# Kernel optimization log

Measured on AMD Instinct MI355X. Metric: run time of the kernel, lower is better.

Reference implementation:

```python
import jax, jax.numpy as jnp
import numpy as np

N_IN = 4_194_304   # len(x)
E = 33_554_432     # len(ptrs) == len(csr)
N_OUT = 4_194_304  # csr[-1] + 1


def setup_inputs() -> dict:
    key = jax.random.key(0)
    kx, kp, kc = jax.random.split(key, 3)
    x = jax.random.normal(kx, (N_IN,), dtype=jnp.float32)
    ptrs = jax.random.randint(kp, (E,), 0, N_IN, dtype=jnp.int32)
    csr = jnp.sort(jax.random.randint(kc, (E,), 0, N_OUT, dtype=jnp.int32))
    # guarantee csr[-1] + 1 == N_OUT (output buffer size in the torch module)
    csr = csr.at[0].set(0).at[-1].set(N_OUT - 1)
    return {"x": x, "ptrs": ptrs, "csr": csr}


def reference(x, ptrs, csr):
    # gather by ptrs, then segment-sum by sorted csr ids into N_OUT buckets
    return jax.ops.segment_sum(x[ptrs], csr, num_segments=N_OUT,
                               indices_are_sorted=True)
```

## Files before the change

kernel.cpp:

```cpp
#include <hip/hip_runtime.h>
#include <hip/hip_fp16.h>


typedef int   v4i __attribute__((ext_vector_type(4)));
typedef float v4f __attribute__((ext_vector_type(4)));

#define VPT   16
#define BLOCK 256

__global__ __launch_bounds__(BLOCK) void x_to_f16_kernel(
    const float* __restrict__ x, __half* __restrict__ xh)
{
    const int i = (blockIdx.x * BLOCK + threadIdx.x) * 8;
    const v4f* src = reinterpret_cast<const v4f*>(x + i);
    v4f a = __builtin_nontemporal_load(src);
    v4f b = __builtin_nontemporal_load(src + 1);
    union { __half h[8]; v4i v; } u;
#pragma unroll
    for (int k = 0; k < 4; ++k) u.h[k]     = __float2half(a[k]);
#pragma unroll
    for (int k = 0; k < 4; ++k) u.h[4 + k] = __float2half(b[k]);
    *reinterpret_cast<v4i*>(xh + i) = u.v;
}

__global__ __launch_bounds__(BLOCK) void seg_sum_f16_kernel(
    const __half* __restrict__ xh,
    const int*    __restrict__ ptrs,
    const int*    __restrict__ csr,
    float*        __restrict__ out)
{
    const long long tid  = (long long)blockIdx.x * BLOCK + threadIdx.x;
    const long long base = tid * VPT;

    const v4i* p4 = reinterpret_cast<const v4i*>(ptrs + base);
    const v4i* c4 = reinterpret_cast<const v4i*>(csr  + base);

    v4i p[VPT / 4], c[VPT / 4];
#pragma unroll
    for (int q = 0; q < VPT / 4; ++q) {
        p[q] = __builtin_nontemporal_load(p4 + q);
        c[q] = __builtin_nontemporal_load(c4 + q);
    }

    int pi[VPT], ci[VPT];
#pragma unroll
    for (int q = 0; q < VPT / 4; ++q) {
#pragma unroll
        for (int k = 0; k < 4; ++k) {
            pi[4 * q + k] = p[q][k];
            ci[4 * q + k] = c[q][k];
        }
    }

    float v[VPT];
#pragma unroll
    for (int j = 0; j < VPT; ++j) v[j] = __half2float(xh[pi[j]]);

    float acc = v[0];
    int   cur = ci[0];
#pragma unroll
    for (int j = 1; j < VPT; ++j) {
        if (ci[j] == cur) {
            acc += v[j];
        } else {
            atomicAdd(&out[cur], acc);
            cur = ci[j];
            acc = v[j];
        }
    }
    atomicAdd(&out[cur], acc);
}

__global__ __launch_bounds__(BLOCK) void seg_sum_f32_kernel(
    const float* __restrict__ x,
    const int*   __restrict__ ptrs,
    const int*   __restrict__ csr,
    float*       __restrict__ out)
{
    const long long tid  = (long long)blockIdx.x * BLOCK + threadIdx.x;
    const long long base = tid * VPT;
    const v4i* p4 = reinterpret_cast<const v4i*>(ptrs + base);
    const v4i* c4 = reinterpret_cast<const v4i*>(csr  + base);
    v4i p[VPT / 4], c[VPT / 4];
#pragma unroll
    for (int q = 0; q < VPT / 4; ++q) {
        p[q] = __builtin_nontemporal_load(p4 + q);
        c[q] = __builtin_nontemporal_load(c4 + q);
    }
    int pi[VPT], ci[VPT];
#pragma unroll
    for (int q = 0; q < VPT / 4; ++q) {
#pragma unroll
        for (int k = 0; k < 4; ++k) { pi[4*q+k] = p[q][k]; ci[4*q+k] = c[q][k]; }
    }
    float v[VPT];
#pragma unroll
    for (int j = 0; j < VPT; ++j) v[j] = x[pi[j]];
    float acc = v[0];
    int   cur = ci[0];
#pragma unroll
    for (int j = 1; j < VPT; ++j) {
        if (ci[j] == cur) { acc += v[j]; }
        else { atomicAdd(&out[cur], acc); cur = ci[j]; acc = v[j]; }
    }
    atomicAdd(&out[cur], acc);
}

extern "C" void kernel_launch(void* const* d_in, const int* in_sizes, int n_in,
                              void* d_out, int out_size, void* d_ws, size_t ws_size,
                              hipStream_t stream) {
    const float* x    = (const float*)d_in[0];
    const int*   ptrs = (const int*)d_in[1];
    const int*   csr  = (const int*)d_in[2];
    float*       out  = (float*)d_out;

    const int n_in_elems = in_sizes[0];
    const int e          = in_sizes[1];
    const int threads    = e / VPT;
    const int grid       = threads / BLOCK;

    hipMemsetAsync(d_out, 0, (size_t)out_size * sizeof(float), stream);

    const size_t xh_bytes = (size_t)n_in_elems * sizeof(__half);
    if (ws_size >= xh_bytes) {
        __half* xh = (__half*)d_ws;
        x_to_f16_kernel<<<n_in_elems / (BLOCK * 8), BLOCK, 0, stream>>>(x, xh);
        seg_sum_f16_kernel<<<grid, BLOCK, 0, stream>>>(xh, ptrs, csr, out);
    } else {
        seg_sum_f32_kernel<<<grid, BLOCK, 0, stream>>>(x, ptrs, csr, out);
    }
}
```

Before: 391.3 us.

## Split gather into two passes over x halves with XCD-aware block remapping

Runs the gather-and-segment-sum kernel twice, each pass only gathering the entries whose pointer falls in one half of the fp16 x array, so the working set of random gathers is smaller and more likely to stay in cache. Blocks are remapped so that consecutive chunks land on the same XCD, improving L2 locality for the streamed index arrays. In exchange, ptrs and csr are read twice from HBM and the number of atomics can nearly double, since each segment may emit one atomic per pass.

New measurement: 454.6 us. +16.2%, slower.

```diff
diff --git a/kernel.cpp b/kernel.cpp
--- a/kernel.cpp
+++ b/kernel.cpp
@@ -7,6 +7,8 @@
 
 #define VPT   16
 #define BLOCK 256
+#define NPASS 2
+#define NXCD  8
 
 __global__ __launch_bounds__(BLOCK) void x_to_f16_kernel(
     const float* __restrict__ x, __half* __restrict__ xh)
@@ -23,14 +25,18 @@
     *reinterpret_cast<v4i*>(xh + i) = u.v;
 }
 
-__global__ __launch_bounds__(BLOCK) void seg_sum_f16_kernel(
+__global__ __launch_bounds__(BLOCK) void seg_sum_pass_kernel(
     const __half* __restrict__ xh,
     const int*    __restrict__ ptrs,
     const int*    __restrict__ csr,
-    float*        __restrict__ out)
+    float*        __restrict__ out,
+    int lo, unsigned wsize)
 {
-    const long long tid  = (long long)blockIdx.x * BLOCK + threadIdx.x;
-    const long long base = tid * VPT;
+    const int nb    = gridDim.x;
+    const int bid   = blockIdx.x;
+    const int chunk = (bid & (NXCD - 1)) * (nb / NXCD) + (bid / NXCD);
+
+    const long long base = ((long long)chunk * BLOCK + threadIdx.x) * VPT;
 
     const v4i* p4 = reinterpret_cast<const v4i*>(ptrs + base);
     const v4i* c4 = reinterpret_cast<const v4i*>(csr  + base);
@@ -52,23 +58,29 @@
         }
     }
 
+    bool  in[VPT];
     float v[VPT];
 #pragma unroll
-    for (int j = 0; j < VPT; ++j) v[j] = __half2float(xh[pi[j]]);
+    for (int j = 0; j < VPT; ++j)
+        in[j] = ((unsigned)(pi[j] - lo) < wsize);
+#pragma unroll
+    for (int j = 0; j < VPT; ++j)
+        v[j] = in[j] ? __half2float(xh[pi[j]]) : 0.0f;
 
-    float acc = v[0];
+    float acc = 0.0f;
     int   cur = ci[0];
+    bool  any = false;
 #pragma unroll
-    for (int j = 1; j < VPT; ++j) {
-        if (ci[j] == cur) {
-            acc += v[j];
-        } else {
-            atomicAdd(&out[cur], acc);
+    for (int j = 0; j < VPT; ++j) {
+        if (ci[j] != cur) {
+            if (any) atomicAdd(&out[cur], acc);
             cur = ci[j];
-            acc = v[j];
+            acc = 0.0f;
+            any = false;
         }
+        if (in[j]) { acc += v[j]; any = true; }
     }
-    atomicAdd(&out[cur], acc);
+    if (any) atomicAdd(&out[cur], acc);
 }
 
 __global__ __launch_bounds__(BLOCK) void seg_sum_f32_kernel(
@@ -122,10 +134,14 @@
     hipMemsetAsync(d_out, 0, (size_t)out_size * sizeof(float), stream);
 
     const size_t xh_bytes = (size_t)n_in_elems * sizeof(__half);
-    if (ws_size >= xh_bytes) {
+    if (ws_size >= xh_bytes && (grid % NXCD) == 0) {
         __half* xh = (__half*)d_ws;
         x_to_f16_kernel<<<n_in_elems / (BLOCK * 8), BLOCK, 0, stream>>>(x, xh);
-        seg_sum_f16_kernel<<<grid, BLOCK, 0, stream>>>(xh, ptrs, csr, out);
+        const unsigned wsize = (unsigned)(n_in_elems / NPASS);
+        for (int pass = 0; pass < NPASS; ++pass) {
+            seg_sum_pass_kernel<<<grid, BLOCK, 0, stream>>>(
+                xh, ptrs, csr, out, pass * (int)wsize, wsize);
+        }
     } else {
         seg_sum_f32_kernel<<<grid, BLOCK, 0, stream>>>(x, ptrs, csr, out);
     }
```

## Double per-thread work and remap blocks to XCD-contiguous chunks in fp16 segsum

Applied to the files above, without the earlier changes.

Each thread in the fp16 path now handles 32 edges instead of 16, halving the grid. Blocks are remapped so that blocks landing on the same XCD (round-robin dispatch) process contiguous ranges of ptrs/csr, aiming to improve L2 locality of output atomics and cross-block segment boundaries. Gathers now load raw ushort values and convert lazily. Register pressure doubles, which can lower occupancy and reduce gather latency hiding.

New measurement: 474.9 us. 1.21x slower.

```diff
diff --git a/kernel.cpp b/kernel.cpp
--- a/kernel.cpp
+++ b/kernel.cpp
@@ -5,8 +5,10 @@
 typedef int   v4i __attribute__((ext_vector_type(4)));
 typedef float v4f __attribute__((ext_vector_type(4)));
 
-#define VPT   16
+#define VPT   32
+#define HALF_VPT 16
 #define BLOCK 256
+#define NXCD  8
 
 __global__ __launch_bounds__(BLOCK) void x_to_f16_kernel(
     const float* __restrict__ x, __half* __restrict__ xh)
@@ -29,11 +31,16 @@
     const int*    __restrict__ csr,
     float*        __restrict__ out)
 {
-    const long long tid  = (long long)blockIdx.x * BLOCK + threadIdx.x;
-    const long long base = tid * VPT;
+    const int nb    = gridDim.x;
+    const int bid   = blockIdx.x;
+    const int chunk = (bid & (NXCD - 1)) * (nb / NXCD) + (bid / NXCD);
+
+    const long long base = ((long long)chunk * BLOCK + threadIdx.x) * VPT;
 
     const v4i* p4 = reinterpret_cast<const v4i*>(ptrs + base);
     const v4i* c4 = reinterpret_cast<const v4i*>(csr  + base);
+    const unsigned short* __restrict__ xu =
+        reinterpret_cast<const unsigned short*>(xh);
 
     v4i p[VPT / 4], c[VPT / 4];
 #pragma unroll
@@ -52,20 +59,21 @@
         }
     }
 
-    float v[VPT];
+    unsigned short h[VPT];
 #pragma unroll
-    for (int j = 0; j < VPT; ++j) v[j] = __half2float(xh[pi[j]]);
+    for (int j = 0; j < VPT; ++j) h[j] = xu[pi[j]];
 
-    float acc = v[0];
+    float acc = __half2float(__ushort_as_half(h[0]));
     int   cur = ci[0];
 #pragma unroll
     for (int j = 1; j < VPT; ++j) {
+        const float vj = __half2float(__ushort_as_half(h[j]));
         if (ci[j] == cur) {
-            acc += v[j];
+            acc += vj;
         } else {
             atomicAdd(&out[cur], acc);
             cur = ci[j];
-            acc = v[j];
+            acc = vj;
         }
     }
     atomicAdd(&out[cur], acc);
@@ -78,28 +86,28 @@
     float*       __restrict__ out)
 {
     const long long tid  = (long long)blockIdx.x * BLOCK + threadIdx.x;
-    const long long base = tid * VPT;
+    const long long base = tid * HALF_VPT;
     const v4i* p4 = reinterpret_cast<const v4i*>(ptrs + base);
     const v4i* c4 = reinterpret_cast<const v4i*>(csr  + base);
-    v4i p[VPT / 4], c[VPT / 4];
+    v4i p[HALF_VPT / 4], c[HALF_VPT / 4];
 #pragma unroll
-    for (int q = 0; q < VPT / 4; ++q) {
+    for (int q = 0; q < HALF_VPT / 4; ++q) {
         p[q] = __builtin_nontemporal_load(p4 + q);
         c[q] = __builtin_nontemporal_load(c4 + q);
     }
-    int pi[VPT], ci[VPT];
+    int pi[HALF_VPT], ci[HALF_VPT];
 #pragma unroll
-    for (int q = 0; q < VPT / 4; ++q) {
+    for (int q = 0; q < HALF_VPT / 4; ++q) {
 #pragma unroll
         for (int k = 0; k < 4; ++k) { pi[4*q+k] = p[q][k]; ci[4*q+k] = c[q][k]; }
     }
-    float v[VPT];
+    float v[HALF_VPT];
 #pragma unroll
-    for (int j = 0; j < VPT; ++j) v[j] = x[pi[j]];
+    for (int j = 0; j < HALF_VPT; ++j) v[j] = x[pi[j]];
     float acc = v[0];
     int   cur = ci[0];
 #pragma unroll
-    for (int j = 1; j < VPT; ++j) {
+    for (int j = 1; j < HALF_VPT; ++j) {
         if (ci[j] == cur) { acc += v[j]; }
         else { atomicAdd(&out[cur], acc); cur = ci[j]; acc = v[j]; }
     }
@@ -116,17 +124,17 @@
 
     const int n_in_elems = in_sizes[0];
     const int e          = in_sizes[1];
-    const int threads    = e / VPT;
-    const int grid       = threads / BLOCK;
 
     hipMemsetAsync(d_out, 0, (size_t)out_size * sizeof(float), stream);
 
     const size_t xh_bytes = (size_t)n_in_elems * sizeof(__half);
-    if (ws_size >= xh_bytes) {
+    const int grid32 = e / (VPT * BLOCK);
+    if (ws_size >= xh_bytes && (grid32 % NXCD) == 0) {
         __half* xh = (__half*)d_ws;
         x_to_f16_kernel<<<n_in_elems / (BLOCK * 8), BLOCK, 0, stream>>>(x, xh);
-        seg_sum_f16_kernel<<<grid, BLOCK, 0, stream>>>(xh, ptrs, csr, out);
+        seg_sum_f16_kernel<<<grid32, BLOCK, 0, stream>>>(xh, ptrs, csr, out);
     } else {
-        seg_sum_f32_kernel<<<grid, BLOCK, 0, stream>>>(x, ptrs, csr, out);
+        seg_sum_f32_kernel<<<e / (HALF_VPT * BLOCK), BLOCK, 0, stream>>>(
+            x, ptrs, csr, out);
     }
 }
```
